# Kernel optimization log

Hardware: AMD Instinct MI355X
Metric: run time of the kernel (lower is better)

Reference implementation:

```python
import math
import jax, jax.numpy as jnp
import numpy as np

H = 1024
N = 64
DT_MIN, DT_MAX = 0.001, 0.1


def setup_inputs() -> dict:
    key = jax.random.key(0)
    k1, k2 = jax.random.split(key)
    # log_dt ~ Uniform[log(dt_min), log(dt_max)]
    log_dt = jax.random.uniform(k1, (H,), dtype=jnp.float32) * (
        math.log(DT_MAX) - math.log(DT_MIN)) + math.log(DT_MIN)
    # C stored as real view of a complex (H, N/2) tensor: last dim = (real, imag)
    C = jax.random.normal(k2, (H, N // 2, 2), dtype=jnp.float32)
    log_A_real = jnp.log(0.5 * jnp.ones((H, N // 2), dtype=jnp.float32))
    A_imag = math.pi * jnp.broadcast_to(
        jnp.arange(N // 2, dtype=jnp.float32)[None, :], (H, N // 2))
    return {"log_dt": log_dt, "C": C, "log_A_real": log_A_real,
            "A_imag": A_imag, "L": 4096}


def reference(log_dt, C, log_A_real, A_imag, L):
    dt = jnp.exp(log_dt)                                   # (H,)
    Cc = jax.lax.complex(C[..., 0], C[..., 1])             # (H, N/2) complex
    A = -jnp.exp(log_A_real) + 1j * A_imag                 # (H, N/2) complex
    dtA = A * dt[:, None]                                  # (H, N/2)
    t = jnp.arange(L, dtype=jnp.float32)                   # (L,)
    K = dtA[:, :, None] * t                                # (H, N/2, L) complex
    Cc = Cc * (jnp.exp(dtA) - 1.0) / A                     # (H, N/2)
    # contract over state dim n; take real part, times 2 (conjugate-pair halves)
    kernel = 2.0 * jnp.einsum('hn,hnl->hl', Cc, jnp.exp(K)).real  # (H, L)
    return kernel
```

## Files before the change

kernel.cpp:

```cpp
#include <hip/hip_runtime.h>


#define NN  32
#define LL  4096
#define TPB 256
#define HPB 2
#define TPH (TPB/HPB)
#define CH  (LL/TPH)

typedef float f32x2 __attribute__((ext_vector_type(2)));

__global__ __launch_bounds__(TPB, 2) void s4d_kernel(
    const float* __restrict__ log_dt,
    const float* __restrict__ C,
    const float* __restrict__ log_A_real,
    const float* __restrict__ A_imag,
    float* __restrict__ out)
{
    const int h0   = blockIdx.x * HPB;
    const int t    = threadIdx.x;
    const int sub  = t / TPH;
    const int lane = t % TPH;
    const int h    = h0 + sub;

    __shared__ float  s_cr[HPB][NN], s_ci[HPB][NN];
    __shared__ float  s_dtAre[HPB][NN];
    __shared__ double s_rev[HPB][NN];
    __shared__ float  s_Wr[HPB][NN], s_Wi[HPB][NN];
    __shared__ float  s_a[HPB][NN], s_m[HPB][NN];

    if (t < HPB * NN) {
        const int ss = t / NN;
        const int n  = t % NN;
        const int hh = h0 + ss;
        const float dt    = __expf(log_dt[hh]);
        const float Are   = -__expf(log_A_real[hh * NN + n]);
        const float Aim   = A_imag[hh * NN + n];
        const float dtAre = dt * Are;
        const float dtAim = dt * Aim;

        const float e = __expf(dtAre);
        float s, c;
        __sincosf(dtAim, &s, &c);
        const float nre = e * c - 1.0f;
        const float nim = e * s;
        const float inv = 1.0f / (Are * Are + Aim * Aim);
        const float fre = (nre * Are + nim * Aim) * inv;
        const float fim = (nim * Are - nre * Aim) * inv;

        const float Cre = C[(hh * NN + n) * 2 + 0];
        const float Cim = C[(hh * NN + n) * 2 + 1];
        s_cr[ss][n] = Cre * fre - Cim * fim;
        s_ci[ss][n] = Cre * fim + Cim * fre;
        s_dtAre[ss][n] = dtAre;

        const double rev1 = (double)dt * (double)Aim * 0.15915494309189535;
        s_rev[ss][n] = rev1;

        double rw = rev1 * (double)TPH;
        rw -= floor(rw);
        float sw, cw;
        __sincosf((float)rw * 6.2831853071795864f, &sw, &cw);
        const float ew = __expf(dtAre * (float)TPH);
        const float Wr = ew * cw, Wi = ew * sw;
        s_Wr[ss][n] = Wr;
        s_Wi[ss][n] = Wi;
        s_a[ss][n]  = 2.0f * Wr;
        s_m[ss][n]  = ew * ew;
    }
    __syncthreads();

    f32x2 acc[CH];
#pragma unroll
    for (int i = 0; i < CH; ++i) acc[i] = (f32x2){0.0f, 0.0f};

    const float lf = (float)lane;

    for (int np = 0; np < NN; np += 2) {
        float x0[2], x1[2];
#pragma unroll
        for (int j = 0; j < 2; ++j) {
            const int n = np + j;
            double rv = s_rev[sub][n] * (double)lane;
            rv -= floor(rv);
            float si, ci;
            __sincosf((float)rv * 6.2831853071795864f, &si, &ci);
            const float er = __expf(s_dtAre[sub][n] * lf);
            const float zr = er * ci, zi = er * si;
            const float cr = s_cr[sub][n], cim = s_ci[sub][n];
            const float xr0 = cr * zr - cim * zi;
            const float xi0 = cr * zi + cim * zr;
            x0[j] = xr0;
            x1[j] = xr0 * s_Wr[sub][n] - xi0 * s_Wi[sub][n];
        }
        const f32x2 a2 = { s_a[sub][np],  s_a[sub][np + 1] };
        const f32x2 m2 = { -s_m[sub][np], -s_m[sub][np + 1] };
        f32x2 xp = { x0[0], x0[1] };
        f32x2 xc = { x1[0], x1[1] };
#pragma unroll
        for (int i = 0; i < CH; i += 2) {
            acc[i]     += xp;
            acc[i + 1] += xc;
            xp = __builtin_elementwise_fma(a2, xc, m2 * xp);
            xc = __builtin_elementwise_fma(a2, xp, m2 * xc);
        }
    }

    float* o = out + (size_t)h * LL + lane;
#pragma unroll
    for (int i = 0; i < CH; ++i)
        o[(size_t)i * TPH] = 2.0f * (acc[i].x + acc[i].y);
}

extern "C" void kernel_launch(void* const* d_in, const int* in_sizes, int n_in,
                              void* d_out, int out_size, void* d_ws, size_t ws_size,
                              hipStream_t stream) {
    const float* log_dt     = (const float*)d_in[0];
    const float* C          = (const float*)d_in[1];
    const float* log_A_real = (const float*)d_in[2];
    const float* A_imag     = (const float*)d_in[3];
    float* out = (float*)d_out;

    const int H = in_sizes[0];
    s4d_kernel<<<dim3(H / HPB), dim3(TPB), 0, stream>>>(log_dt, C, log_A_real, A_imag, out);
}
```

Baseline: 76.81 us.

## Split state dimension across two thread halves per head with smem reduction

Each block now handles one head, and its two 128-thread halves each process half of the 32 state modes. Partial sums are combined through a shared-memory reduction before the store. The recurrence is reworked into four interleaved chains (even/odd, stride-2 blocks) stepped with V=W^2, giving more independent FMA chains per mode. Launch bounds rise to 4 blocks per SM. The cost is an extra reduction, a sync, and more shared-memory traffic; the per-thread accumulator count is unchanged.

```diff
diff --git a/kernel.cpp b/kernel.cpp
--- a/kernel.cpp
+++ b/kernel.cpp
@@ -4,38 +4,37 @@
 #define NN  32
 #define LL  4096
 #define TPB 256
-#define HPB 2
-#define TPH (TPB/HPB)
+#define TPH 128
 #define CH  (LL/TPH)
+#define NH  16
 
 typedef float f32x2 __attribute__((ext_vector_type(2)));
 
-__global__ __launch_bounds__(TPB, 2) void s4d_kernel(
+__global__ __launch_bounds__(TPB, 4) void s4d_kernel(
     const float* __restrict__ log_dt,
     const float* __restrict__ C,
     const float* __restrict__ log_A_real,
     const float* __restrict__ A_imag,
     float* __restrict__ out)
 {
-    const int h0   = blockIdx.x * HPB;
+    const int h    = blockIdx.x;
     const int t    = threadIdx.x;
-    const int sub  = t / TPH;
-    const int lane = t % TPH;
-    const int h    = h0 + sub;
+    const int half = t >> 7;
+    const int lane = t & (TPH - 1);
 
-    __shared__ float  s_cr[HPB][NN], s_ci[HPB][NN];
-    __shared__ float  s_dtAre[HPB][NN];
-    __shared__ double s_rev[HPB][NN];
-    __shared__ float  s_Wr[HPB][NN], s_Wi[HPB][NN];
-    __shared__ float  s_a[HPB][NN], s_m[HPB][NN];
+    __shared__ float  s_cr[NN], s_ci[NN];
+    __shared__ float  s_dtAre[NN];
+    __shared__ double s_rev[NN];
+    __shared__ float  s_Wr[NN], s_Wi[NN];
+    __shared__ float  s_Vr[NN], s_Vi[NN];
+    __shared__ float  s_aV[NN], s_mVn[NN];
+    __shared__ float  s_red[TPH][NN + 1];
 
-    if (t < HPB * NN) {
-        const int ss = t / NN;
-        const int n  = t % NN;
-        const int hh = h0 + ss;
-        const float dt    = __expf(log_dt[hh]);
-        const float Are   = -__expf(log_A_real[hh * NN + n]);
-        const float Aim   = A_imag[hh * NN + n];
+    if (t < NN) {
+        const int n = t;
+        const float dt    = __expf(log_dt[h]);
+        const float Are   = -__expf(log_A_real[h * NN + n]);
+        const float Aim   = A_imag[h * NN + n];
         const float dtAre = dt * Are;
         const float dtAim = dt * Aim;
 
@@ -48,25 +47,32 @@
         const float fre = (nre * Are + nim * Aim) * inv;
         const float fim = (nim * Are - nre * Aim) * inv;
 
-        const float Cre = C[(hh * NN + n) * 2 + 0];
-        const float Cim = C[(hh * NN + n) * 2 + 1];
-        s_cr[ss][n] = Cre * fre - Cim * fim;
-        s_ci[ss][n] = Cre * fim + Cim * fre;
-        s_dtAre[ss][n] = dtAre;
+        const float Cre = C[(h * NN + n) * 2 + 0];
+        const float Cim = C[(h * NN + n) * 2 + 1];
+        s_cr[n] = Cre * fre - Cim * fim;
+        s_ci[n] = Cre * fim + Cim * fre;
+        s_dtAre[n] = dtAre;
 
         const double rev1 = (double)dt * (double)Aim * 0.15915494309189535;
-        s_rev[ss][n] = rev1;
+        s_rev[n] = rev1;
 
         double rw = rev1 * (double)TPH;
         rw -= floor(rw);
         float sw, cw;
         __sincosf((float)rw * 6.2831853071795864f, &sw, &cw);
         const float ew = __expf(dtAre * (float)TPH);
-        const float Wr = ew * cw, Wi = ew * sw;
-        s_Wr[ss][n] = Wr;
-        s_Wi[ss][n] = Wi;
-        s_a[ss][n]  = 2.0f * Wr;
-        s_m[ss][n]  = ew * ew;
+        s_Wr[n] = ew * cw;
+        s_Wi[n] = ew * sw;
+
+        double rv2 = rev1 * (double)(2 * TPH);
+        rv2 -= floor(rv2);
+        float sv, cv;
+        __sincosf((float)rv2 * 6.2831853071795864f, &sv, &cv);
+        const float ew2 = ew * ew;
+        s_Vr[n]  = ew2 * cv;
+        s_Vi[n]  = ew2 * sv;
+        s_aV[n]  = 2.0f * (ew2 * cv);
+        s_mVn[n] = -(ew2 * ew2);
     }
     __syncthreads();
 
@@ -74,42 +80,61 @@
 #pragma unroll
     for (int i = 0; i < CH; ++i) acc[i] = (f32x2){0.0f, 0.0f};
 
-    const float lf = (float)lane;
+    const float lf    = (float)lane;
+    const int   nbase = half * NH;
 
-    for (int np = 0; np < NN; np += 2) {
-        float x0[2], x1[2];
+    for (int j0 = 0; j0 < NH; j0 += 2) {
+        const int np = nbase + j0;
+        float E0[2], E1[2], O0[2], O1[2];
 #pragma unroll
-        for (int j = 0; j < 2; ++j) {
-            const int n = np + j;
-            double rv = s_rev[sub][n] * (double)lane;
+        for (int jj = 0; jj < 2; ++jj) {
+            const int n = np + jj;
+            double rv = s_rev[n] * (double)lane;
             rv -= floor(rv);
-            float si, ci;
-            __sincosf((float)rv * 6.2831853071795864f, &si, &ci);
-            const float er = __expf(s_dtAre[sub][n] * lf);
-            const float zr = er * ci, zi = er * si;
-            const float cr = s_cr[sub][n], cim = s_ci[sub][n];
-            const float xr0 = cr * zr - cim * zi;
-            const float xi0 = cr * zi + cim * zr;
-            x0[j] = xr0;
-            x1[j] = xr0 * s_Wr[sub][n] - xi0 * s_Wi[sub][n];
+            float si, co;
+            __sincosf((float)rv * 6.2831853071795864f, &si, &co);
+            const float er = __expf(s_dtAre[n] * lf);
+            const float zr = er * co, zi = er * si;
+            const float cr = s_cr[n], cim = s_ci[n];
+            const float xr = cr * zr - cim * zi;
+            const float xi = cr * zi + cim * zr;
+            const float Wr = s_Wr[n], Wi = s_Wi[n];
+            const float x1r = xr * Wr - xi * Wi;
+            const float x1i = xr * Wi + xi * Wr;
+            const float Vr = s_Vr[n], Vi = s_Vi[n];
+            E0[jj] = xr;
+            E1[jj] = xr * Vr - xi * Vi;
+            O0[jj] = x1r;
+            O1[jj] = x1r * Vr - x1i * Vi;
         }
-        const f32x2 a2 = { s_a[sub][np],  s_a[sub][np + 1] };
-        const f32x2 m2 = { -s_m[sub][np], -s_m[sub][np + 1] };
-        f32x2 xp = { x0[0], x0[1] };
-        f32x2 xc = { x1[0], x1[1] };
+        const f32x2 aV  = { s_aV[np],  s_aV[np + 1] };
+        const f32x2 mVn = { s_mVn[np], s_mVn[np + 1] };
+        f32x2 e0 = { E0[0], E0[1] }, e1 = { E1[0], E1[1] };
+        f32x2 o0 = { O0[0], O0[1] }, o1 = { O1[0], O1[1] };
 #pragma unroll
-        for (int i = 0; i < CH; i += 2) {
-            acc[i]     += xp;
-            acc[i + 1] += xc;
-            xp = __builtin_elementwise_fma(a2, xc, m2 * xp);
-            xc = __builtin_elementwise_fma(a2, xp, m2 * xc);
+        for (int i = 0; i < CH; i += 4) {
+            acc[i]     += e0;
+            acc[i + 1] += o0;
+            acc[i + 2] += e1;
+            acc[i + 3] += o1;
+            e0 = __builtin_elementwise_fma(aV, e1, mVn * e0);
+            o0 = __builtin_elementwise_fma(aV, o1, mVn * o0);
+            e1 = __builtin_elementwise_fma(aV, e0, mVn * e1);
+            o1 = __builtin_elementwise_fma(aV, o0, mVn * o1);
         }
     }
 
-    float* o = out + (size_t)h * LL + lane;
+    const int io = (1 - half) * NH;
+    const int is = half * NH;
 #pragma unroll
-    for (int i = 0; i < CH; ++i)
-        o[(size_t)i * TPH] = 2.0f * (acc[i].x + acc[i].y);
+    for (int k = 0; k < NH; ++k)
+        s_red[lane][io + k] = acc[io + k].x + acc[io + k].y;
+    __syncthreads();
+
+    float* o = out + (size_t)h * LL + (size_t)is * TPH + lane;
+#pragma unroll
+    for (int k = 0; k < NH; ++k)
+        o[(size_t)k * TPH] = 2.0f * (acc[is + k].x + acc[is + k].y + s_red[lane][is + k]);
 }
 
 extern "C" void kernel_launch(void* const* d_in, const int* in_sizes, int n_in,
@@ -122,5 +147,5 @@
     float* out = (float*)d_out;
 
     const int H = in_sizes[0];
-    s4d_kernel<<<dim3(H / HPB), dim3(TPB), 0, stream>>>(log_dt, C, log_A_real, A_imag, out);
+    s4d_kernel<<<dim3(H), dim3(TPB), 0, stream>>>(log_dt, C, log_A_real, A_imag, out);
 }
```

Result: slower. 102.1 us (+32.9%).
